# Kernel optimization log

Hardware: AMD Instinct MI355X
Metric: run time of the kernel (lower is better)

## Reference

```python
import jax, jax.numpy as jnp
import numpy as np

B, T, S, A, H = 64, 1000, 96, 32, 256
INP = S + A  # 128


def setup_inputs() -> dict:
    key = jax.random.key(0)
    ks = jax.random.split(key, 20)
    def xavier(k, shape):
        fan_in, fan_out = shape[0], shape[1]
        lim = jnp.sqrt(6.0 / (fan_in + fan_out))
        return jax.random.uniform(k, shape, jnp.float32, -lim, lim)
    return {
        "state": jax.random.normal(ks[0], (B, T, S), jnp.float32),
        "action": jax.random.normal(ks[1], (B, T, A), jnp.float32),
        "hn": jnp.zeros((1, B, H), jnp.float32),
        # branch 1 params
        "fc11_w": xavier(ks[2], (INP, H)),
        "fc11_b": jnp.zeros((H,), jnp.float32),
        "W_hh1": xavier(ks[3], (H, H)),
        "W_ih1": xavier(ks[4], (H, H)),
        "b_hh1": jax.random.uniform(ks[5], (H,), jnp.float32),
        "b_ih1": jax.random.uniform(ks[6], (H,), jnp.float32),
        "fc12_w": xavier(ks[7], (H, 1)),
        "fc12_b": jnp.zeros((1,), jnp.float32),
        # branch 2 params
        "fc21_w": xavier(ks[8], (INP, H)),
        "fc21_b": jnp.zeros((H,), jnp.float32),
        "W_hh2": xavier(ks[9], (H, H)),
        "W_ih2": xavier(ks[10], (H, H)),
        "b_hh2": jax.random.uniform(ks[11], (H,), jnp.float32),
        "b_ih2": jax.random.uniform(ks[12], (H,), jnp.float32),
        "fc22_w": xavier(ks[13], (H, 1)),
        "fc22_b": jnp.zeros((1,), jnp.float32),
    }


def _rnn_branch(x, h0, W_hh, W_ih, b_hh, b_ih):
    # x: [B, T, H] (post input projection + relu); h0: [B, H]
    bias = b_hh + b_ih
    def step(h, x_t):
        h_next = jax.nn.sigmoid(h @ W_hh + x_t @ W_ih + bias)
        return h_next, h_next
    xs = jnp.swapaxes(x, 0, 1)  # [T, B, H]
    _, hs = jax.lax.scan(step, h0, xs)
    return jnp.swapaxes(hs, 0, 1)  # [B, T, H]


def reference(state, action, hn, fc11_w, fc11_b, W_hh1, W_ih1, b_hh1, b_ih1,
              fc12_w, fc12_b, fc21_w, fc21_b, W_hh2, W_ih2, b_hh2, b_ih2,
              fc22_w, fc22_b):
    x = jnp.concatenate((state, action), axis=-1)  # [B, T, INP]
    h0 = hn[0]  # squeeze(0) -> [B, H]

    x1 = jax.nn.relu(x @ fc11_w + fc11_b)
    rnn1 = _rnn_branch(x1, h0, W_hh1, W_ih1, b_hh1, b_ih1)
    q1 = rnn1 @ fc12_w + fc12_b  # [B, T, 1]

    x2 = jax.nn.relu(x @ fc21_w + fc21_b)
    rnn2 = _rnn_branch(x2, h0, W_hh2, W_ih2, b_hh2, b_ih2)
    q2 = rnn2 @ fc22_w + fc22_b  # [B, T, 1]

    return (q1, q2)
```

## Files before the change

### kernel.cpp

```cpp
#include <hip/hip_runtime.h>
#include <math.h>


typedef _Float16 half2_t __attribute__((ext_vector_type(2)));
typedef __attribute__((ext_vector_type(8))) short bf16x8;
typedef __attribute__((ext_vector_type(4))) float f32x4;

__device__ __forceinline__ float fdot2(half2_t a, half2_t b, float c) {
#if __has_builtin(__builtin_amdgcn_fdot2)
    return __builtin_amdgcn_fdot2(a, b, c, false);
#else
    return c + (float)a[0] * (float)b[0] + (float)a[1] * (float)b[1];
#endif
}

__device__ __forceinline__ short f2bf(float f) {
    unsigned u = __builtin_bit_cast(unsigned, f);
    return (short)((u + 0x7FFFu + ((u >> 16) & 1u)) >> 16);
}

__device__ __forceinline__ void barrier_lds() {
    __asm__ __volatile__("s_waitcnt lgkmcnt(0)" ::: "memory");
    __builtin_amdgcn_s_barrier();
}

__global__ __launch_bounds__(256, 1)
void prep_kernel(const float* __restrict__ fc11_w, const float* __restrict__ W_ih1,
                 const float* __restrict__ fc21_w, const float* __restrict__ W_ih2,
                 short* __restrict__ tab)
{
    const int e    = blockIdx.x * 256 + threadIdx.x;
    const int lane = e & 63;
    const int q = lane >> 4, m = lane & 15;
    const float* W;
    int k0, n;
    if (e < 8192) {
        int t_ = e >> 6;
        int ks = t_ & 3, nt = (t_ >> 2) & 15, br = t_ >> 6;
        W = br ? fc21_w : fc11_w;
        k0 = ks * 32 + q * 8; n = nt * 16 + m;
    } else {
        int t_ = (e - 8192) >> 6;
        int ks = t_ & 7, nt = (t_ >> 3) & 15, br = t_ >> 7;
        W = br ? W_ih2 : W_ih1;
        k0 = ks * 32 + q * 8; n = nt * 16 + m;
    }
    bf16x8 v;
#pragma unroll
    for (int j = 0; j < 8; ++j) v[j] = f2bf(W[(size_t)(k0 + j) * 256 + n]);
    ((bf16x8*)tab)[e] = v;
}

__global__ __launch_bounds__(256, 2)
void ff_kernel(const float* __restrict__ state,
               const float* __restrict__ action,
               const float* __restrict__ fc11_b, const float* __restrict__ fc21_b,
               const float* __restrict__ b_hh1, const float* __restrict__ b_ih1,
               const float* __restrict__ b_hh2, const float* __restrict__ b_ih2,
               const short* __restrict__ tab,
               _Float16* __restrict__ pre_out)
{
    __shared__ short X1[128 * 264];

    const int tile = blockIdx.x % 500;
    const int br   = blockIdx.x / 500;
    const int tid  = threadIdx.x;
    const int w    = tid >> 6;
    const int lane = tid & 63;
    const int q = lane >> 4, m = lane & 15;
    const int row0 = tile * 128;

    const float* ba = br ? fc21_b : fc11_b;
    const float* bh = br ? b_hh2 : b_hh1;
    const float* bi = br ? b_ih2 : b_ih1;
    const bf16x8* tG1 = (const bf16x8*)tab + (size_t)br * 4096;
    const bf16x8* tG2 = (const bf16x8*)tab + 8192 + (size_t)br * 8192;

    float ba_v[16], bb_v[16];
#pragma unroll
    for (int nt = 0; nt < 16; ++nt) {
        int c = nt * 16 + m;
        ba_v[nt] = ba[c];
        bb_v[nt] = bh[c] + bi[c];
    }

    bf16x8 af[2][4];
#pragma unroll
    for (int mt = 0; mt < 2; ++mt) {
        const int rw = row0 + 64 * mt + 16 * w + m;
#pragma unroll
        for (int ks = 0; ks < 4; ++ks) {
            int k0 = ks * 32 + q * 8;
            const float* src = (k0 < 96) ? (state  + (size_t)rw * 96 + k0)
                                         : (action + (size_t)rw * 32 + (k0 - 96));
            float4 x0 = *(const float4*)src;
            float4 x1 = *(const float4*)(src + 4);
            bf16x8 a;
            a[0] = f2bf(x0.x); a[1] = f2bf(x0.y); a[2] = f2bf(x0.z); a[3] = f2bf(x0.w);
            a[4] = f2bf(x1.x); a[5] = f2bf(x1.y); a[6] = f2bf(x1.z); a[7] = f2bf(x1.w);
            af[mt][ks] = a;
        }
    }

#pragma unroll 4
    for (int nt = 0; nt < 16; ++nt) {
        bf16x8 bf[4];
#pragma unroll
        for (int ks = 0; ks < 4; ++ks) bf[ks] = tG1[(nt * 4 + ks) * 64 + lane];
#pragma unroll
        for (int mt = 0; mt < 2; ++mt) {
            f32x4 acc = {0.f, 0.f, 0.f, 0.f};
#pragma unroll
            for (int ks = 0; ks < 4; ++ks)
                acc = __builtin_amdgcn_mfma_f32_16x16x32_bf16(af[mt][ks], bf[ks], acc, 0, 0, 0);
#pragma unroll
            for (int r = 0; r < 4; ++r) {
                float v = acc[r] + ba_v[nt];
                v = v > 0.f ? v : 0.f;
                X1[(64 * mt + 16 * w + q * 4 + r) * 264 + nt * 16 + m] = f2bf(v);
            }
        }
    }

    bf16x8 a2[2][8];
#pragma unroll
    for (int mt = 0; mt < 2; ++mt)
#pragma unroll
        for (int ks = 0; ks < 8; ++ks)
            a2[mt][ks] = *(const bf16x8*)&X1[(64 * mt + 16 * w + m) * 264 + ks * 32 + q * 8];

    _Float16* pre = pre_out + (size_t)br * 64000u * 256u;
#pragma unroll 2
    for (int nt = 0; nt < 16; ++nt) {
        bf16x8 bg[8];
#pragma unroll
        for (int ks = 0; ks < 8; ++ks) bg[ks] = tG2[(nt * 8 + ks) * 64 + lane];
#pragma unroll
        for (int mt = 0; mt < 2; ++mt) {
            f32x4 acc = {0.f, 0.f, 0.f, 0.f};
#pragma unroll
            for (int ks = 0; ks < 8; ++ks)
                acc = __builtin_amdgcn_mfma_f32_16x16x32_bf16(a2[mt][ks], bg[ks], acc, 0, 0, 0);
#pragma unroll
            for (int r = 0; r < 4; ++r) {
                float v = acc[r] + bb_v[nt];
                pre[(size_t)(row0 + 64 * mt + 16 * w + q * 4 + r) * 256 + nt * 16 + m] = (_Float16)v;
            }
        }
    }
}

__global__ __launch_bounds__(256)
__attribute__((amdgpu_waves_per_eu(1, 1)))
void rnn_kernel(const _Float16* __restrict__ pre_all,
                const float* __restrict__ hn,
                const float* __restrict__ W_hh1,
                const float* __restrict__ W_hh2,
                _Float16* __restrict__ h_out)
{
    __shared__ _Float16 hbuf[256];
    __shared__ float part[2][4][256];

    const int wg = blockIdx.x;
    const int br = wg >> 6;
    const int b  = wg & 63;
    const float* Whh = br ? W_hh2 : W_hh1;
    const _Float16* pre = pre_all + ((size_t)br * 64000u + (size_t)b * 1000u) * 256u;
    _Float16* hg = h_out + ((size_t)br * 64000u + (size_t)b * 1000u) * 256u;

    const int t  = threadIdx.x;
    const int w  = t >> 6;
    const int l  = t & 63;
    const int k0 = w * 64;
    const int c0 = l * 4;

    unsigned whb[4][32];
#pragma unroll
    for (int i = 0; i < 32; ++i) {
        float4 lo = *(const float4*)(Whh + (size_t)(k0 + 2 * i) * 256 + c0);
        float4 hi = *(const float4*)(Whh + (size_t)(k0 + 2 * i + 1) * 256 + c0);
        whb[0][i] = __builtin_bit_cast(unsigned, half2_t{(_Float16)lo.x, (_Float16)hi.x});
        whb[1][i] = __builtin_bit_cast(unsigned, half2_t{(_Float16)lo.y, (_Float16)hi.y});
        whb[2][i] = __builtin_bit_cast(unsigned, half2_t{(_Float16)lo.z, (_Float16)hi.z});
        whb[3][i] = __builtin_bit_cast(unsigned, half2_t{(_Float16)lo.w, (_Float16)hi.w});
    }
#pragma unroll
    for (int c = 0; c < 4; ++c)
#pragma unroll
        for (int i = 0; i < 32; ++i)
            __asm__ __volatile__("" : "+v"(whb[c][i]));

    hbuf[t] = (_Float16)hn[b * 256 + t];
    barrier_lds();

    float pre_c = (float)pre[t];
    float pre_n = (float)pre[256 + t];

    for (int tt = 0; tt < 1000; ++tt) {
        const int t2 = (tt + 2 < 1000) ? (tt + 2) : 999;
        const float pre_n2 = (float)pre[(size_t)t2 * 256 + t];

        const float4* hb = (const float4*)&hbuf[k0];
        float sA0 = 0.f, sA1 = 0.f, sA2 = 0.f, sA3 = 0.f;
        float sB0 = 0.f, sB1 = 0.f, sB2 = 0.f, sB3 = 0.f;
#pragma unroll
        for (int k = 0; k < 8; ++k) {
            float4 v = hb[k];
            const half2_t* hh = (const half2_t*)&v;
#define WH(c, idx) __builtin_bit_cast(half2_t, whb[c][idx])
            sA0 = fdot2(hh[0], WH(0, 4 * k + 0), sA0);
            sA1 = fdot2(hh[0], WH(1, 4 * k + 0), sA1);
            sA2 = fdot2(hh[0], WH(2, 4 * k + 0), sA2);
            sA3 = fdot2(hh[0], WH(3, 4 * k + 0), sA3);
            sA0 = fdot2(hh[1], WH(0, 4 * k + 1), sA0);
            sA1 = fdot2(hh[1], WH(1, 4 * k + 1), sA1);
            sA2 = fdot2(hh[1], WH(2, 4 * k + 1), sA2);
            sA3 = fdot2(hh[1], WH(3, 4 * k + 1), sA3);
            sB0 = fdot2(hh[2], WH(0, 4 * k + 2), sB0);
            sB1 = fdot2(hh[2], WH(1, 4 * k + 2), sB1);
            sB2 = fdot2(hh[2], WH(2, 4 * k + 2), sB2);
            sB3 = fdot2(hh[2], WH(3, 4 * k + 2), sB3);
            sB0 = fdot2(hh[3], WH(0, 4 * k + 3), sB0);
            sB1 = fdot2(hh[3], WH(1, 4 * k + 3), sB1);
            sB2 = fdot2(hh[3], WH(2, 4 * k + 3), sB2);
            sB3 = fdot2(hh[3], WH(3, 4 * k + 3), sB3);
#undef WH
        }
        const int pp = tt & 1;
        *(float4*)&part[pp][w][c0] =
            float4{sA0 + sB0, sA1 + sB1, sA2 + sB2, sA3 + sB3};
        barrier_lds();

        const float z = ((part[pp][0][t] + part[pp][1][t]) +
                         (part[pp][2][t] + part[pp][3][t])) + pre_c;
        const float h = 1.0f / (1.0f + __expf(-z));
        const _Float16 h16 = (_Float16)h;
        hbuf[t] = h16;
        hg[(size_t)tt * 256 + t] = h16;

        pre_c = pre_n;
        pre_n = pre_n2;
    }
}

__global__ __launch_bounds__(256, 2)
void q_kernel(const _Float16* __restrict__ h_all,
              const float* __restrict__ fc12_w, const float* __restrict__ fc12_b,
              const float* __restrict__ fc22_w, const float* __restrict__ fc22_b,
              float* __restrict__ out)
{
    const int n  = blockIdx.x * 256 + threadIdx.x;
    const int br = (n >= 64000);
    const float* qwp = br ? fc22_w : fc12_w;
    const float  qb  = br ? fc22_b[0] : fc12_b[0];

    half2_t qw[128];
#pragma unroll
    for (int i = 0; i < 128; ++i)
        qw[i] = half2_t{(_Float16)qwp[2 * i], (_Float16)qwp[2 * i + 1]};

    const float4* hr = (const float4*)(h_all + (size_t)n * 256u);
    float s0 = qb, s1 = 0.f, s2 = 0.f, s3 = 0.f;
#pragma unroll
    for (int k = 0; k < 32; ++k) {
        float4 v = hr[k];
        const half2_t* hh = (const half2_t*)&v;
        s0 = fdot2(hh[0], qw[4 * k + 0], s0);
        s1 = fdot2(hh[1], qw[4 * k + 1], s1);
        s2 = fdot2(hh[2], qw[4 * k + 2], s2);
        s3 = fdot2(hh[3], qw[4 * k + 3], s3);
    }
    out[n] = (s0 + s1) + (s2 + s3);
}

extern "C" void kernel_launch(void* const* d_in, const int* in_sizes, int n_in,
                              void* d_out, int out_size, void* d_ws, size_t ws_size,
                              hipStream_t stream)
{
    const float* state  = (const float*)d_in[0];
    const float* action = (const float*)d_in[1];
    const float* hn     = (const float*)d_in[2];
    const float* fc11_w = (const float*)d_in[3];
    const float* fc11_b = (const float*)d_in[4];
    const float* W_hh1  = (const float*)d_in[5];
    const float* W_ih1  = (const float*)d_in[6];
    const float* b_hh1  = (const float*)d_in[7];
    const float* b_ih1  = (const float*)d_in[8];
    const float* fc12_w = (const float*)d_in[9];
    const float* fc12_b = (const float*)d_in[10];
    const float* fc21_w = (const float*)d_in[11];
    const float* fc21_b = (const float*)d_in[12];
    const float* W_hh2  = (const float*)d_in[13];
    const float* W_ih2  = (const float*)d_in[14];
    const float* b_hh2  = (const float*)d_in[15];
    const float* b_ih2  = (const float*)d_in[16];
    const float* fc22_w = (const float*)d_in[17];
    const float* fc22_b = (const float*)d_in[18];

    _Float16* pre = (_Float16*)d_ws;
    _Float16* hbg = (_Float16*)d_ws + 32768000u;
    short* tab = (short*)((char*)d_ws + 130678784u);

    prep_kernel<<<96, 256, 0, stream>>>(fc11_w, W_ih1, fc21_w, W_ih2, tab);
    ff_kernel<<<1000, 256, 0, stream>>>(state, action,
                                        fc11_b, fc21_b, b_hh1, b_ih1,
                                        b_hh2, b_ih2, tab, pre);
    rnn_kernel<<<128, 256, 0, stream>>>(pre, hn, W_hh1, W_hh2, hbg);
    q_kernel<<<500, 256, 0, stream>>>(hbg, fc12_w, fc12_b, fc22_w, fc22_b,
                                      (float*)d_out);
}
```

Measured before the change: 756.8 us.

## Split RNN recurrence reduction across eight waves per block

Each RNN block now uses 512 threads (8 waves) instead of 256. Each wave owns a 32-row slice of the hidden-state reduction instead of 64, so every thread runs half as many dependent fdot2 steps per timestep. The price is eight partial sums per output column instead of four, a wider barrier, and an epilogue in which only half of each wave's lanes compute the sigmoid. The aim is to shorten the serial per-step latency of the recurrence, which is the critical path.

```diff
diff --git a/kernel.cpp b/kernel.cpp
--- a/kernel.cpp
+++ b/kernel.cpp
@@ -150,8 +150,7 @@
     }
 }
 
-__global__ __launch_bounds__(256)
-__attribute__((amdgpu_waves_per_eu(1, 1)))
+__global__ __launch_bounds__(512, 2)
 void rnn_kernel(const _Float16* __restrict__ pre_all,
                 const float* __restrict__ hn,
                 const float* __restrict__ W_hh1,
@@ -159,7 +158,7 @@
                 _Float16* __restrict__ h_out)
 {
     __shared__ _Float16 hbuf[256];
-    __shared__ float part[2][4][256];
+    __shared__ float part[2][8][256];
 
     const int wg = blockIdx.x;
     const int br = wg >> 6;
@@ -168,15 +167,16 @@
     const _Float16* pre = pre_all + ((size_t)br * 64000u + (size_t)b * 1000u) * 256u;
     _Float16* hg = h_out + ((size_t)br * 64000u + (size_t)b * 1000u) * 256u;
 
-    const int t  = threadIdx.x;
-    const int w  = t >> 6;
-    const int l  = t & 63;
-    const int k0 = w * 64;
-    const int c0 = l * 4;
-
-    unsigned whb[4][32];
-#pragma unroll
-    for (int i = 0; i < 32; ++i) {
+    const int t    = threadIdx.x;
+    const int w    = t >> 6;
+    const int lane = t & 63;
+    const int k0   = w * 32;
+    const int c0   = lane * 4;
+    const int cr   = (w << 5) + (lane & 31);
+
+    unsigned whb[4][16];
+#pragma unroll
+    for (int i = 0; i < 16; ++i) {
         float4 lo = *(const float4*)(Whh + (size_t)(k0 + 2 * i) * 256 + c0);
         float4 hi = *(const float4*)(Whh + (size_t)(k0 + 2 * i + 1) * 256 + c0);
         whb[0][i] = __builtin_bit_cast(unsigned, half2_t{(_Float16)lo.x, (_Float16)hi.x});
@@ -187,56 +187,49 @@
 #pragma unroll
     for (int c = 0; c < 4; ++c)
 #pragma unroll
-        for (int i = 0; i < 32; ++i)
+        for (int i = 0; i < 16; ++i)
             __asm__ __volatile__("" : "+v"(whb[c][i]));
 
-    hbuf[t] = (_Float16)hn[b * 256 + t];
+    if (t < 256) hbuf[t] = (_Float16)hn[b * 256 + t];
     barrier_lds();
 
-    float pre_c = (float)pre[t];
-    float pre_n = (float)pre[256 + t];
+    float pre_c = (float)pre[cr];
+    float pre_n = (float)pre[256 + cr];
 
     for (int tt = 0; tt < 1000; ++tt) {
         const int t2 = (tt + 2 < 1000) ? (tt + 2) : 999;
-        const float pre_n2 = (float)pre[(size_t)t2 * 256 + t];
+        const float pre_n2 = (float)pre[(size_t)t2 * 256 + cr];
 
         const float4* hb = (const float4*)&hbuf[k0];
-        float sA0 = 0.f, sA1 = 0.f, sA2 = 0.f, sA3 = 0.f;
-        float sB0 = 0.f, sB1 = 0.f, sB2 = 0.f, sB3 = 0.f;
-#pragma unroll
-        for (int k = 0; k < 8; ++k) {
+        float s0 = 0.f, s1 = 0.f, s2 = 0.f, s3 = 0.f;
+#pragma unroll
+        for (int k = 0; k < 4; ++k) {
             float4 v = hb[k];
             const half2_t* hh = (const half2_t*)&v;
 #define WH(c, idx) __builtin_bit_cast(half2_t, whb[c][idx])
-            sA0 = fdot2(hh[0], WH(0, 4 * k + 0), sA0);
-            sA1 = fdot2(hh[0], WH(1, 4 * k + 0), sA1);
-            sA2 = fdot2(hh[0], WH(2, 4 * k + 0), sA2);
-            sA3 = fdot2(hh[0], WH(3, 4 * k + 0), sA3);
-            sA0 = fdot2(hh[1], WH(0, 4 * k + 1), sA0);
-            sA1 = fdot2(hh[1], WH(1, 4 * k + 1), sA1);
-            sA2 = fdot2(hh[1], WH(2, 4 * k + 1), sA2);
-            sA3 = fdot2(hh[1], WH(3, 4 * k + 1), sA3);
-            sB0 = fdot2(hh[2], WH(0, 4 * k + 2), sB0);
-            sB1 = fdot2(hh[2], WH(1, 4 * k + 2), sB1);
-            sB2 = fdot2(hh[2], WH(2, 4 * k + 2), sB2);
-            sB3 = fdot2(hh[2], WH(3, 4 * k + 2), sB3);
-            sB0 = fdot2(hh[3], WH(0, 4 * k + 3), sB0);
-            sB1 = fdot2(hh[3], WH(1, 4 * k + 3), sB1);
-            sB2 = fdot2(hh[3], WH(2, 4 * k + 3), sB2);
-            sB3 = fdot2(hh[3], WH(3, 4 * k + 3), sB3);
+#pragma unroll
+            for (int p = 0; p < 4; ++p) {
+                s0 = fdot2(hh[p], WH(0, 4 * k + p), s0);
+                s1 = fdot2(hh[p], WH(1, 4 * k + p), s1);
+                s2 = fdot2(hh[p], WH(2, 4 * k + p), s2);
+                s3 = fdot2(hh[p], WH(3, 4 * k + p), s3);
+            }
 #undef WH
         }
         const int pp = tt & 1;
-        *(float4*)&part[pp][w][c0] =
-            float4{sA0 + sB0, sA1 + sB1, sA2 + sB2, sA3 + sB3};
+        *(float4*)&part[pp][w][c0] = float4{s0, s1, s2, s3};
         barrier_lds();
 
-        const float z = ((part[pp][0][t] + part[pp][1][t]) +
-                         (part[pp][2][t] + part[pp][3][t])) + pre_c;
-        const float h = 1.0f / (1.0f + __expf(-z));
-        const _Float16 h16 = (_Float16)h;
-        hbuf[t] = h16;
-        hg[(size_t)tt * 256 + t] = h16;
+        if (lane < 32) {
+            const float* pc = &part[pp][0][cr];
+            float z = ((pc[0 * 256] + pc[1 * 256]) + (pc[2 * 256] + pc[3 * 256]))
+                    + ((pc[4 * 256] + pc[5 * 256]) + (pc[6 * 256] + pc[7 * 256]))
+                    + pre_c;
+            const float h = 1.0f / (1.0f + __expf(-z));
+            const _Float16 h16 = (_Float16)h;
+            hbuf[cr] = h16;
+            hg[(size_t)tt * 256 + cr] = h16;
+        }
 
         pre_c = pre_n;
         pre_n = pre_n2;
@@ -305,7 +298,7 @@
     ff_kernel<<<1000, 256, 0, stream>>>(state, action,
                                         fc11_b, fc21_b, b_hh1, b_ih1,
                                         b_hh2, b_ih2, tab, pre);
-    rnn_kernel<<<128, 256, 0, stream>>>(pre, hn, W_hh1, W_hh2, hbg);
+    rnn_kernel<<<128, 512, 0, stream>>>(pre, hn, W_hh1, W_hh2, hbg);
     q_kernel<<<500, 256, 0, stream>>>(hbg, fc12_w, fc12_b, fc22_w, fc22_b,
                                       (float*)d_out);
 }
```

Result: no change. 764.0 us (+1.0%).
